# Performance work log

Hardware: AMD Instinct MI355X
Metric: run time of the kernel (lower is better)

Reference implementation:

```python
import jax, jax.numpy as jnp
import numpy as np

EPS = 1e-5

def _bn(x, g, b, m, v):
    inv = g / jnp.sqrt(v + EPS)
    return x * inv[None, :, None, None] + (b - m * inv)[None, :, None, None]

def _box_conv(x, y_min, y_max, x_min, x_max):
    # Learnable box filter via integral image + bilinear-interpolated corners.
    # x: (N, C, H, W); box params: (C, B). Output: (N, C*B, H, W), area-normalized.
    N, C, H, W = x.shape
    B = y_min.shape[1]
    # padded integral image (N, C, H+1, W+1)
    I = jnp.pad(jnp.cumsum(jnp.cumsum(x, axis=2), axis=3), ((0, 0), (0, 0), (1, 0), (1, 0)))
    iy = jnp.arange(H, dtype=x.dtype)
    ix = jnp.arange(W, dtype=x.dtype)

    def one_box(Ic, ymn, ymx, xmn, xmx):
        # Ic: (N, H+1, W+1); scalar box extents
        y1 = jnp.clip(iy + ymn, 0.0, H)
        y2 = jnp.clip(iy + ymx + 1.0, 0.0, H)
        x1 = jnp.clip(ix + xmn, 0.0, W)
        x2 = jnp.clip(ix + xmx + 1.0, 0.0, W)

        def interp_y(c):  # (H,) -> (N, H, W+1)
            i0 = jnp.clip(jnp.floor(c), 0.0, H - 1).astype(jnp.int32)
            t = (c - i0)[None, :, None]
            return Ic[:, i0, :] * (1.0 - t) + Ic[:, i0 + 1, :] * t

        Gy1, Gy2 = interp_y(y1), interp_y(y2)

        def interp_x(G, c):  # (N, H, W+1), (W,) -> (N, H, W)
            i0 = jnp.clip(jnp.floor(c), 0.0, W - 1).astype(jnp.int32)
            t = (c - i0)[None, None, :]
            return G[:, :, i0] * (1.0 - t) + G[:, :, i0 + 1] * t

        S = interp_x(Gy2, x2) - interp_x(Gy2, x1) - interp_x(Gy1, x2) + interp_x(Gy1, x1)
        area = (ymx - ymn + 1.0) * (xmx - xmn + 1.0)
        return S / area  # (N, H, W)

    f_b = jax.vmap(one_box, in_axes=(None, 0, 0, 0, 0))   # over boxes
    f_cb = jax.vmap(f_b, in_axes=(1, 0, 0, 0, 0))          # over channels
    out = f_cb(I, y_min, y_max, x_min, x_max)              # (C, B, N, H, W)
    return jnp.transpose(out, (2, 0, 1, 3, 4)).reshape(N, C * B, H, W)


def setup_inputs() -> dict:
    key = jax.random.key(0)
    ks = jax.random.split(key, 20)
    N, Cin, H, W = 32, 256, 56, 56
    Cmid, B = 16, 4
    Cbox = Cmid * B
    Cout = 256
    f32 = jnp.float32
    x = jax.random.normal(ks[0], (N, Cin, H, W), f32)
    w1 = jax.random.normal(ks[1], (Cmid, Cin), f32) * 0.05
    g1 = jax.random.uniform(ks[2], (Cmid,), f32, 0.5, 1.5)
    b1 = jax.random.normal(ks[3], (Cmid,), f32) * 0.1
    m1 = jax.random.normal(ks[4], (Cmid,), f32) * 0.1
    v1 = jax.random.uniform(ks[5], (Cmid,), f32, 0.5, 1.5)
    y_min = -jax.random.uniform(ks[6], (Cmid, B), f32) * 10.0
    y_max = jax.random.uniform(ks[7], (Cmid, B), f32) * 10.0
    x_min = -jax.random.uniform(ks[8], (Cmid, B), f32) * 10.0
    x_max = jax.random.uniform(ks[9], (Cmid, B), f32) * 10.0
    g2 = jax.random.uniform(ks[10], (Cbox,), f32, 0.5, 1.5)
    b2 = jax.random.normal(ks[11], (Cbox,), f32) * 0.1
    m2 = jax.random.normal(ks[12], (Cbox,), f32) * 0.1
    v2 = jax.random.uniform(ks[13], (Cbox,), f32, 0.5, 1.5)
    w3 = jax.random.normal(ks[14], (Cout, Cbox), f32) * 0.05
    g3 = jax.random.uniform(ks[15], (Cout,), f32, 0.5, 1.5)
    b3 = jax.random.normal(ks[16], (Cout,), f32) * 0.1
    m3 = jax.random.normal(ks[17], (Cout,), f32) * 0.1
    v3 = jax.random.uniform(ks[18], (Cout,), f32, 0.5, 1.5)
    return {"x": x, "w1": w1, "g1": g1, "b1": b1, "m1": m1, "v1": v1,
            "y_min": y_min, "y_max": y_max, "x_min": x_min, "x_max": x_max,
            "g2": g2, "b2": b2, "m2": m2, "v2": v2,
            "w3": w3, "g3": g3, "b3": b3, "m3": m3, "v3": v3}


def reference(x, w1, g1, b1, m1, v1, y_min, y_max, x_min, x_max,
              g2, b2, m2, v2, w3, g3, b3, m3, v3):
    out = jnp.einsum('nchw,oc->nohw', x, w1)            # 1x1 conv
    out = jax.nn.relu(_bn(out, g1, b1, m1, v1))
    out = _box_conv(out, y_min, y_max, x_min, x_max)    # (N, Cmid*B, H, W)
    out = jax.nn.relu(_bn(out, g2, b2, m2, v2))
    out = jnp.einsum('nchw,oc->nohw', out, w3)          # 1x1 conv
    out = _bn(out, g3, b3, m3, v3)
    return jax.nn.relu(out + x)
```

## Files before the change

kernel.cpp:

```cpp
#include <hip/hip_runtime.h>
#include <hip/hip_bf16.h>
#include <math.h>

#define EPSB 1e-5f

constexpr int NN = 32, CIN = 256, HH = 56, WW = 56, HW = HH * WW;
constexpr int CMID = 16, NB = 4, CBOX = 64, COUT = 256;

typedef __attribute__((ext_vector_type(8))) short short8;
typedef __attribute__((ext_vector_type(4))) float f32x4;

constexpr size_t WS_OUT1  = 0;
constexpr size_t WS_OUT2B = WS_OUT1 + (size_t)NN * CMID * HW;

__global__ __launch_bounds__(256) void k1(const float* __restrict__ x,
                                          const float* __restrict__ w1,
                                          const float* __restrict__ g1,
                                          const float* __restrict__ b1,
                                          const float* __restrict__ m1,
                                          const float* __restrict__ v1,
                                          float* __restrict__ out1) {
  __shared__ float w1s[CIN][CMID];
  __shared__ float red[4 * 64 * 17];
  int bid = blockIdx.x;
  int n = bid / 49, hwb = (bid % 49) * 64;
  int tid = threadIdx.x;
  int lane = tid & 63;
  int kq = tid >> 6;
  int kq_u = __builtin_amdgcn_readfirstlane(tid) >> 6;

#pragma unroll
  for (int c = 0; c < CMID; ++c) {
    float inv = g1[c] / sqrtf(v1[c] + EPSB);
    w1s[tid][c] = w1[c * CIN + tid] * inv;
  }
  __syncthreads();

  const float* xb = x + (size_t)n * CIN * HW + hwb + lane;
  float acc[CMID];
#pragma unroll
  for (int c = 0; c < CMID; ++c) acc[c] = 0.f;

  int ci0 = kq_u * 64;
#pragma unroll 8
  for (int i = 0; i < 64; ++i) {
    int ci = ci0 + i;
    float xv = xb[(size_t)ci * HW];
    const f32x4* wv = (const f32x4*)&w1s[ci][0];
#pragma unroll
    for (int q = 0; q < 4; ++q) {
      f32x4 wq = wv[q];
      acc[q * 4 + 0] = fmaf(xv, wq.x, acc[q * 4 + 0]);
      acc[q * 4 + 1] = fmaf(xv, wq.y, acc[q * 4 + 1]);
      acc[q * 4 + 2] = fmaf(xv, wq.z, acc[q * 4 + 2]);
      acc[q * 4 + 3] = fmaf(xv, wq.w, acc[q * 4 + 3]);
    }
  }
#pragma unroll
  for (int c = 0; c < CMID; ++c) red[kq * 1088 + lane * 17 + c] = acc[c];
  __syncthreads();

#pragma unroll
  for (int j = 0; j < 4; ++j) {
    int o = tid + j * 256;
    int c = o >> 6, pix = o & 63;
    float v = red[pix * 17 + c] + red[1088 + pix * 17 + c] +
              red[2176 + pix * 17 + c] + red[3264 + pix * 17 + c];
    float inv = g1[c] / sqrtf(v1[c] + EPSB);
    v += b1[c] - m1[c] * inv;
    out1[((size_t)n * CMID + c) * HW + hwb + pix] = fmaxf(v, 0.f);
  }
}

__device__ __forceinline__ float bilin(const float* __restrict__ sI, float y, float x) {
  int iy = min((int)y, 55);
  int ix = min((int)x, 55);
  float ty = y - (float)iy;
  float tx = x - (float)ix;
  const float* r = sI + iy * 57 + ix;
  float a = r[0], b = r[1], cc = r[57], d = r[58];
  float g1v = a * (1.f - ty) + cc * ty;
  float g2v = b * (1.f - ty) + d * ty;
  return g1v * (1.f - tx) + g2v * tx;
}

__global__ __launch_bounds__(512) void k2(
    const float* __restrict__ out1,
    const float* __restrict__ y_min, const float* __restrict__ y_max,
    const float* __restrict__ x_min, const float* __restrict__ x_max,
    const float* __restrict__ g2, const float* __restrict__ b2,
    const float* __restrict__ m2, const float* __restrict__ v2,
    __hip_bfloat16* __restrict__ out2b) {
  __shared__ float sI[57 * 57];
  int bid = blockIdx.x;
  int n = bid >> 4, c = bid & 15;
  int tid = threadIdx.x;
  int lane = tid & 63, w = tid >> 6;

  if (tid < 57) { sI[tid] = 0.f; sI[tid * 57] = 0.f; }
  const float* src = out1 + ((size_t)n * CMID + c) * HW;
  for (int vdx = tid; vdx < HW / 4; vdx += 512) {
    int p = vdx * 4;
    int h = p / 56, wq = p - h * 56;
    f32x4 d = ((const f32x4*)src)[vdx];
    float* dst = &sI[(h + 1) * 57 + wq + 1];
    dst[0] = d.x; dst[1] = d.y; dst[2] = d.z; dst[3] = d.w;
  }
  __syncthreads();

  for (int r = w; r < 56; r += 8) {
    float* row = &sI[(r + 1) * 57 + 1];
    float vv = (lane < 56) ? row[lane] : 0.f;
#pragma unroll
    for (int d = 1; d < 64; d <<= 1) {
      float o = __shfl_up(vv, d, 64);
      if (lane >= d) vv += o;
    }
    if (lane < 56) row[lane] = vv;
  }
  __syncthreads();
  for (int cc = w; cc < 56; cc += 8) {
    float* col = &sI[57 + cc + 1];
    float vv = (lane < 56) ? col[lane * 57] : 0.f;
#pragma unroll
    for (int d = 1; d < 64; d <<= 1) {
      float o = __shfl_up(vv, d, 64);
      if (lane >= d) vv += o;
    }
    if (lane < 56) col[lane * 57] = vv;
  }
  __syncthreads();

  float pymn[NB], pymx[NB], pxmn[NB], pxmx[NB], pinv[NB], pbi[NB], prar[NB];
#pragma unroll
  for (int b = 0; b < NB; ++b) {
    int cb = c * NB + b;
    pymn[b] = y_min[cb]; pymx[b] = y_max[cb];
    pxmn[b] = x_min[cb]; pxmx[b] = x_max[cb];
    float inv = g2[cb] / sqrtf(v2[cb] + EPSB);
    pinv[b] = inv;
    pbi[b] = b2[cb] - m2[cb] * inv;
    prar[b] = 1.f / ((pymx[b] - pymn[b] + 1.f) * (pxmx[b] - pxmn[b] + 1.f));
  }
  __hip_bfloat16* dst0 = out2b + ((size_t)n * CBOX + c * NB) * HW;

  for (int p = tid; p < HW; p += 512) {
    int h = p / 56, wq = p - h * 56;
    float fh = (float)h, fw = (float)wq;
#pragma unroll
    for (int b = 0; b < NB; ++b) {
      float y1 = fminf(fmaxf(fh + pymn[b], 0.f), 56.f);
      float y2 = fminf(fmaxf(fh + pymx[b] + 1.f, 0.f), 56.f);
      float x1 = fminf(fmaxf(fw + pxmn[b], 0.f), 56.f);
      float x2 = fminf(fmaxf(fw + pxmx[b] + 1.f, 0.f), 56.f);
      float S = bilin(sI, y2, x2) - bilin(sI, y2, x1) - bilin(sI, y1, x2) + bilin(sI, y1, x1);
      float val = S * prar[b] * pinv[b] + pbi[b];
      dst0[(size_t)b * HW + p] = __float2bfloat16(fmaxf(val, 0.f));
    }
  }
}

__global__ __launch_bounds__(512) void k3(
    const __hip_bfloat16* __restrict__ out2b,
    const float* __restrict__ w3,
    const float* __restrict__ g3, const float* __restrict__ b3,
    const float* __restrict__ m3, const float* __restrict__ v3,
    const float* __restrict__ x, float* __restrict__ out) {
  __shared__ __hip_bfloat16 T[64][72];
  int bid = blockIdx.x;
  int n = bid / 49, hwb = (bid % 49) * 64;
  int tid = threadIdx.x;
  int l = tid & 63, w = tid >> 6;

  {
    const __hip_bfloat16* srcp = out2b + ((size_t)n * CBOX + l) * HW + hwb + w * 8;
    short8 v = *reinterpret_cast<const short8*>(srcp);
    const __hip_bfloat16* vp = (const __hip_bfloat16*)&v;
#pragma unroll
    for (int i = 0; i < 8; ++i) T[w * 8 + i][l] = vp[i];
  }

  short8 afrag[2][2];
#pragma unroll
  for (int ot = 0; ot < 2; ++ot)
#pragma unroll
    for (int kh = 0; kh < 2; ++kh) {
      int o = w * 32 + ot * 16 + (l & 15);
      int k0 = kh * 32 + (l >> 4) * 8;
      const float* wp = w3 + o * CBOX + k0;
      union { short8 s; __hip_bfloat16 h[8]; } u;
#pragma unroll
      for (int j = 0; j < 8; ++j) u.h[j] = __float2bfloat16(wp[j]);
      afrag[ot][kh] = u.s;
    }

  __syncthreads();

  short8 bfrag[4][2];
#pragma unroll
  for (int pt = 0; pt < 4; ++pt)
#pragma unroll
    for (int kh = 0; kh < 2; ++kh) {
      int pix = pt * 16 + (l & 15);
      int k0 = kh * 32 + (l >> 4) * 8;
      bfrag[pt][kh] = *reinterpret_cast<const short8*>(&T[pix][k0]);
    }

  f32x4 acc[2][4];
#pragma unroll
  for (int ot = 0; ot < 2; ++ot)
#pragma unroll
    for (int pt = 0; pt < 4; ++pt) acc[ot][pt] = (f32x4)(0.f);

#pragma unroll
  for (int ot = 0; ot < 2; ++ot)
#pragma unroll
    for (int pt = 0; pt < 4; ++pt) {
      acc[ot][pt] = __builtin_amdgcn_mfma_f32_16x16x32_bf16(
          afrag[ot][0], bfrag[pt][0], acc[ot][pt], 0, 0, 0);
      acc[ot][pt] = __builtin_amdgcn_mfma_f32_16x16x32_bf16(
          afrag[ot][1], bfrag[pt][1], acc[ot][pt], 0, 0, 0);
    }

  size_t nbase = (size_t)n * COUT * HW + hwb;
#pragma unroll
  for (int ot = 0; ot < 2; ++ot) {
#pragma unroll
    for (int j = 0; j < 4; ++j) {
      int o = w * 32 + ot * 16 + (l >> 4) * 4 + j;
      float iv = g3[o] / sqrtf(v3[o] + EPSB);
      float bb = b3[o] - m3[o] * iv;
      size_t rowbase = nbase + (size_t)o * HW;
#pragma unroll
      for (int pt = 0; pt < 4; ++pt) {
        int pix = pt * 16 + (l & 15);
        float v = acc[ot][pt][j] * iv + bb + x[rowbase + pix];
        out[rowbase + pix] = fmaxf(v, 0.f);
      }
    }
  }
}

extern "C" void kernel_launch(void* const* d_in, const int* in_sizes, int n_in,
                              void* d_out, int out_size, void* d_ws, size_t ws_size,
                              hipStream_t stream) {
  const float* x   = (const float*)d_in[0];
  const float* w1  = (const float*)d_in[1];
  const float* g1  = (const float*)d_in[2];
  const float* b1  = (const float*)d_in[3];
  const float* m1  = (const float*)d_in[4];
  const float* v1  = (const float*)d_in[5];
  const float* ymn = (const float*)d_in[6];
  const float* ymx = (const float*)d_in[7];
  const float* xmn = (const float*)d_in[8];
  const float* xmx = (const float*)d_in[9];
  const float* g2  = (const float*)d_in[10];
  const float* b2  = (const float*)d_in[11];
  const float* m2  = (const float*)d_in[12];
  const float* v2  = (const float*)d_in[13];
  const float* w3  = (const float*)d_in[14];
  const float* g3  = (const float*)d_in[15];
  const float* b3  = (const float*)d_in[16];
  const float* m3  = (const float*)d_in[17];
  const float* v3  = (const float*)d_in[18];

  float* ws  = (float*)d_ws;
  float* out = (float*)d_out;
  __hip_bfloat16* out2b = (__hip_bfloat16*)(ws + WS_OUT2B);

  k1<<<NN * 49, 256, 0, stream>>>(x, w1, g1, b1, m1, v1, ws + WS_OUT1);
  k2<<<NN * CMID, 512, 0, stream>>>(ws + WS_OUT1, ymn, ymx, xmn, xmx,
                                    g2, b2, m2, v2, out2b);
  k3<<<NN * 49, 512, 0, stream>>>(out2b, w3, g3, b3, m3, v3, x, out);
}
```

Before: 90.11 us.

## Replace scalar FMA 1x1 conv in k1 with bf16 MFMA via LDS staging

```diff
diff --git a/kernel.cpp b/kernel.cpp
--- a/kernel.cpp
+++ b/kernel.cpp
@@ -20,55 +20,57 @@
                                           const float* __restrict__ m1,
                                           const float* __restrict__ v1,
                                           float* __restrict__ out1) {
-  __shared__ float w1s[CIN][CMID];
-  __shared__ float red[4 * 64 * 17];
+  __shared__ __hip_bfloat16 Xb[64][264];
+  __shared__ __hip_bfloat16 Wb[16][264];
   int bid = blockIdx.x;
   int n = bid / 49, hwb = (bid % 49) * 64;
   int tid = threadIdx.x;
-  int lane = tid & 63;
-  int kq = tid >> 6;
-  int kq_u = __builtin_amdgcn_readfirstlane(tid) >> 6;
-
-#pragma unroll
-  for (int c = 0; c < CMID; ++c) {
+  int l = tid & 63, w = tid >> 6;
+
+  {
+    int c = tid >> 4, kb = (tid & 15) * 16;
     float inv = g1[c] / sqrtf(v1[c] + EPSB);
-    w1s[tid][c] = w1[c * CIN + tid] * inv;
-  }
-  __syncthreads();
-
-  const float* xb = x + (size_t)n * CIN * HW + hwb + lane;
-  float acc[CMID];
-#pragma unroll
-  for (int c = 0; c < CMID; ++c) acc[c] = 0.f;
-
-  int ci0 = kq_u * 64;
-#pragma unroll 8
-  for (int i = 0; i < 64; ++i) {
-    int ci = ci0 + i;
-    float xv = xb[(size_t)ci * HW];
-    const f32x4* wv = (const f32x4*)&w1s[ci][0];
-#pragma unroll
-    for (int q = 0; q < 4; ++q) {
-      f32x4 wq = wv[q];
-      acc[q * 4 + 0] = fmaf(xv, wq.x, acc[q * 4 + 0]);
-      acc[q * 4 + 1] = fmaf(xv, wq.y, acc[q * 4 + 1]);
-      acc[q * 4 + 2] = fmaf(xv, wq.z, acc[q * 4 + 2]);
-      acc[q * 4 + 3] = fmaf(xv, wq.w, acc[q * 4 + 3]);
-    }
-  }
-#pragma unroll
-  for (int c = 0; c < CMID; ++c) red[kq * 1088 + lane * 17 + c] = acc[c];
-  __syncthreads();
+    const float* wp = w1 + c * CIN + kb;
+#pragma unroll
+    for (int j = 0; j < 16; ++j)
+      Wb[c][kb + j] = __float2bfloat16(wp[j] * inv);
+  }
+
+  {
+    const float* xb = x + (size_t)n * CIN * HW + hwb;
+    int pxq = (tid & 15) * 4;
+    int cio = (tid >> 4) * 2;
+#pragma unroll
+    for (int p = 0; p < 8; ++p) {
+      int ci = p * 32 + cio;
+      f32x4 a = *reinterpret_cast<const f32x4*>(xb + (size_t)ci * HW + pxq);
+      f32x4 b = *reinterpret_cast<const f32x4*>(xb + (size_t)(ci + 1) * HW + pxq);
+#pragma unroll
+      for (int j = 0; j < 4; ++j) {
+        unsigned lo = (unsigned)__bfloat16_as_ushort(__float2bfloat16(a[j]));
+        unsigned hi = (unsigned)__bfloat16_as_ushort(__float2bfloat16(b[j]));
+        *reinterpret_cast<unsigned*>(&Xb[pxq + j][ci]) = lo | (hi << 16);
+      }
+    }
+  }
+  __syncthreads();
+
+  int pix = 16 * w + (l & 15);
+  f32x4 acc = (f32x4)(0.f);
+#pragma unroll
+  for (int kk = 0; kk < 8; ++kk) {
+    int k0 = kk * 32 + (l >> 4) * 8;
+    short8 afr = *reinterpret_cast<const short8*>(&Wb[l & 15][k0]);
+    short8 bfr = *reinterpret_cast<const short8*>(&Xb[pix][k0]);
+    acc = __builtin_amdgcn_mfma_f32_16x16x32_bf16(afr, bfr, acc, 0, 0, 0);
+  }
 
 #pragma unroll
   for (int j = 0; j < 4; ++j) {
-    int o = tid + j * 256;
-    int c = o >> 6, pix = o & 63;
-    float v = red[pix * 17 + c] + red[1088 + pix * 17 + c] +
-              red[2176 + pix * 17 + c] + red[3264 + pix * 17 + c];
+    int c = (l >> 4) * 4 + j;
     float inv = g1[c] / sqrtf(v1[c] + EPSB);
-    v += b1[c] - m1[c] * inv;
-    out1[((size_t)n * CMID + c) * HW + hwb + pix] = fmaxf(v, 0.f);
+    float val = acc[j] + (b1[c] - m1[c] * inv);
+    out1[((size_t)n * CMID + c) * HW + hwb + pix] = fmaxf(val, 0.f);
   }
 }
 
```

Result: faster. 81.52 us (median of 2 runs) (-9.5%).
